# Kernel tuning notes

Measured on AMD Instinct MI355X. Metric: run time of the kernel, lower is better.

The kernel has to match this reference:

```python
import jax, jax.numpy as jnp
import numpy as np

T = 1048576  # length of the return series


def setup_inputs() -> dict:
    key = jax.random.key(0)
    y = jax.random.normal(key, (T,), dtype=jnp.float32) * 0.01
    f32 = lambda v: jnp.asarray(v, dtype=jnp.float32)
    return {
        "y": y,
        "omega": f32(0.000115944368734123),
        "alpha": f32(2.91880490811086e-06),
        "phi": f32(0.887721679393748),
        "lam": f32(2.38788661600365),
        "gam1": f32(332.934927419811),
        "gam2": f32(134.424516082664),
        "vphi": f32(1.61007979938689e-06),
        "rho": f32(0.990486709209338),
    }


def reference(y, omega, alpha, phi, lam, gam1, gam2, vphi, rho):
    # Component Heston-Nandi GARCH volatility recurrence.
    # h_0 = q_0 = Var(y)  (population variance, matching tf.math.reduce_variance)
    q0 = jnp.var(y)
    h0 = q0

    def step(carry, y_prev):
        h_t, q_t = carry
        s = jnp.sqrt(h_t)
        z = (y_prev - lam * h_t) / s
        innov = z * z - 1.0
        q_new = omega + rho * (q_t - omega) + vphi * (innov - 2.0 * gam2 * s * z)
        h_new = q_new + phi * (h_t - q_new) + alpha * (innov - 2.0 * gam1 * s * z)
        return (h_new, q_new), h_new

    # step t uses y[t-1], producing h[1..T-1]
    (_, _), hs = jax.lax.scan(step, (h0, q0), y[:-1])
    return jnp.concatenate([h0[None], hs])  # shape (T,)
```

## Files before the change

### kernel.cpp

```cpp
#include <hip/hip_runtime.h>

#define T_LEN   1048576
#define CHUNK   16
#define WARM    512
#define SBLOCK  256
#define OUTS_PER_BLOCK (SBLOCK * CHUNK)
#define SGRID   (T_LEN / OUTS_PER_BLOCK)
#define WIN     (WARM + OUTS_PER_BLOCK)
#define WIN4    (WIN / 4)
#define LDS_DW  (WIN + (WIN / 64) * 4)
#define RGRID   256

__global__ __launch_bounds__(256)
void var_partials_kernel(const float* __restrict__ y, double2* __restrict__ ws) {
    int tid = blockIdx.x * blockDim.x + threadIdx.x;
    const float4* y4 = (const float4*)y;
    const int stride = RGRID * 256;
    float4 v0 = y4[tid];
    float4 v1 = y4[tid + stride];
    float4 v2 = y4[tid + 2 * stride];
    float4 v3 = y4[tid + 3 * stride];
    double s = 0.0, s2 = 0.0;
    #define ACC(v) { double a=(v).x,b=(v).y,c=(v).z,d=(v).w; s += (a+b)+(c+d); s2 += (a*a+b*b)+(c*c+d*d); }
    ACC(v0) ACC(v1) ACC(v2) ACC(v3)
    #undef ACC
    for (int off = 32; off >= 1; off >>= 1) {
        s  += __shfl_down(s,  off, 64);
        s2 += __shfl_down(s2, off, 64);
    }
    __shared__ double lsum[4], lsq[4];
    int lane = threadIdx.x & 63, wv = threadIdx.x >> 6;
    if (lane == 0) { lsum[wv] = s; lsq[wv] = s2; }
    __syncthreads();
    if (threadIdx.x == 0) {
        double2 o;
        o.x = (lsum[0] + lsum[1]) + (lsum[2] + lsum[3]);
        o.y = (lsq[0]  + lsq[1])  + (lsq[2]  + lsq[3]);
        ws[blockIdx.x] = o;
    }
}

struct ChnP { float lam, DA, E, B, phi, A, cV, rho, cv2, vphi; };

__device__ __forceinline__ void chn_step(float yv, float& h, float& q, const ChnP& P) {
    float u  = fmaf(-P.lam, h, yv);
    float r  = __builtin_amdgcn_rcpf(h);
    float t1 = fmaf(P.E, q, P.DA);
    float s1 = fmaf(P.rho, q, P.cV);
    float u2 = u * u;
    float t2 = fmaf(P.B, u, t1);
    float s2 = fmaf(P.cv2, u, s1);
    float t3 = fmaf(P.phi, h, t2);
    float Ar = P.A * r;
    float Vr = P.vphi * r;
    h = fmaf(u2, Ar, t3);
    q = fmaf(u2, Vr, s2);
}

__device__ __forceinline__ void chn_step4(const float4& v, float& h, float& q, const ChnP& P) {
    chn_step(v.x, h, q, P);
    chn_step(v.y, h, q, P);
    chn_step(v.z, h, q, P);
    chn_step(v.w, h, q, P);
}

__device__ __forceinline__ float4 lds_r4(const float* b, int d) {
    return *(const float4*)&b[d + ((d >> 6) << 2)];
}
__device__ __forceinline__ void lds_w4(float* b, int d, float4 v) {
    *(float4*)&b[d + ((d >> 6) << 2)] = v;
}

__global__ __launch_bounds__(SBLOCK, 1)
void chn_scan_kernel(const float* __restrict__ y, float* __restrict__ out,
                     const double2* __restrict__ ws,
                     const float* __restrict__ p_omega, const float* __restrict__ p_alpha,
                     const float* __restrict__ p_phi,   const float* __restrict__ p_lam,
                     const float* __restrict__ p_gam1,  const float* __restrict__ p_gam2,
                     const float* __restrict__ p_vphi,  const float* __restrict__ p_rho) {
    __shared__ __align__(16) float ybuf[LDS_DW];

    const int B0    = blockIdx.x * OUTS_PER_BLOCK;
    const int gbase = (blockIdx.x == 0) ? 0 : (B0 - WARM);

    {
        const float4* g4 = (const float4*)(y + gbase);
        for (int i = threadIdx.x; i < WIN4; i += SBLOCK) {
            lds_w4(ybuf, 4 * i, g4[i]);
        }
    }

    const float omega = *p_omega, alpha = *p_alpha, phi = *p_phi, lam = *p_lam;
    const float gam1 = *p_gam1, gam2 = *p_gam2, vphi = *p_vphi, rho = *p_rho;
    const float onemphi = 1.0f - phi;
    const float c0  = omega * (1.0f - rho);
    const float cv2 = -2.0f * gam2 * vphi;
    const float c1  = -2.0f * gam1 * alpha;
    ChnP P;
    P.lam = lam; P.rho = rho; P.cv2 = cv2; P.vphi = vphi; P.phi = phi;
    P.A  = fmaf(onemphi, vphi, alpha);
    P.B  = fmaf(onemphi, cv2, c1);
    P.E  = onemphi * rho;
    P.DA = onemphi * c0 - P.A;
    P.cV = c0 - vphi;

    int lane = threadIdx.x & 63;
    double s = 0.0, s2 = 0.0;
    #pragma unroll
    for (int k = 0; k < 4; ++k) {
        double2 v = ws[lane + 64 * k];
        s += v.x; s2 += v.y;
    }
    #pragma unroll
    for (int off = 32; off >= 1; off >>= 1) {
        s  += __shfl_xor(s,  off, 64);
        s2 += __shfl_xor(s2, off, 64);
    }
    const double inv_t = 1.0 / (double)T_LEN;
    double mean = s * inv_t;
    const float var = (float)(s2 * inv_t - mean * mean);

    __syncthreads();

    const int t0 = B0 + threadIdx.x * CHUNK;
    float h = var, q = var;
    float4* out4 = (float4*)(out + t0);

    if (blockIdx.x != 0) {
        const int dw = threadIdx.x * CHUNK;
        float4 a = lds_r4(ybuf, dw + 0);
        float4 b = lds_r4(ybuf, dw + 4);
        #pragma unroll 2
        for (int f = 0; f < WARM / 4; f += 2) {
            float4 na = lds_r4(ybuf, dw + 4 * (f + 2));
            float4 nb = lds_r4(ybuf, dw + 4 * (f + 3));
            chn_step4(a, h, q, P);
            chn_step4(b, h, q, P);
            a = na; b = nb;
        }
        float4 c = lds_r4(ybuf, dw + WARM + 8);
        float4 d = lds_r4(ybuf, dw + WARM + 12);
        float4 o;
        o.x = h; chn_step(a.x, h, q, P);
        o.y = h; chn_step(a.y, h, q, P);
        o.z = h; chn_step(a.z, h, q, P);
        o.w = h; chn_step(a.w, h, q, P);
        out4[0] = o;
        o.x = h; chn_step(b.x, h, q, P);
        o.y = h; chn_step(b.y, h, q, P);
        o.z = h; chn_step(b.z, h, q, P);
        o.w = h; chn_step(b.w, h, q, P);
        out4[1] = o;
        o.x = h; chn_step(c.x, h, q, P);
        o.y = h; chn_step(c.y, h, q, P);
        o.z = h; chn_step(c.z, h, q, P);
        o.w = h; chn_step(c.w, h, q, P);
        out4[2] = o;
        o.x = h; chn_step(d.x, h, q, P);
        o.y = h; chn_step(d.y, h, q, P);
        o.z = h; chn_step(d.z, h, q, P);
        o.w = h; chn_step(d.w, h, q, P);
        out4[3] = o;
    } else {
        const int nW = (t0 < WARM) ? t0 : WARM;
        const int d0 = t0 - nW;
        for (int f = 0; f < nW / 4; ++f) {
            float4 v = lds_r4(ybuf, d0 + 4 * f);
            chn_step4(v, h, q, P);
        }
        #pragma unroll
        for (int j = 0; j < CHUNK / 4; ++j) {
            float4 v = lds_r4(ybuf, t0 + 4 * j);
            float4 o;
            o.x = h; chn_step(v.x, h, q, P);
            o.y = h; chn_step(v.y, h, q, P);
            o.z = h; chn_step(v.z, h, q, P);
            o.w = h; chn_step(v.w, h, q, P);
            out4[j] = o;
        }
    }
}

extern "C" void kernel_launch(void* const* d_in, const int* in_sizes, int n_in,
                              void* d_out, int out_size, void* d_ws, size_t ws_size,
                              hipStream_t stream) {
    const float* y = (const float*)d_in[0];
    float* out = (float*)d_out;
    double2* ws = (double2*)d_ws;

    var_partials_kernel<<<RGRID, 256, 0, stream>>>(y, ws);

    chn_scan_kernel<<<SGRID, SBLOCK, 0, stream>>>(
        y, out, ws,
        (const float*)d_in[1], (const float*)d_in[2], (const float*)d_in[3],
        (const float*)d_in[4], (const float*)d_in[5], (const float*)d_in[6],
        (const float*)d_in[7], (const float*)d_in[8]);
}
```

Before: 89.49 us.

## Fuse variance reduction into scan kernel with cross-block flag sync; shorten warmup

Removes the separate variance-partials kernel. Each scan block now sums its own 4096-element slice from the LDS copy it already loads, publishes the partial sums with a release flag, and spins until all 256 blocks' flags are set before computing the variance. This removes one launch and a second pass over global memory. The warm-up length drops from 512 to 448 steps, which shortens the serial recurrence each thread runs, at some cost in accuracy. The step function also merges the two reciprocal multiplies into one shared product. Risks: the grid-wide spin wait depends on all blocks being co-resident. The flags are never reset, so later calls can read the previous call's partial sums before the current ones are written.

```diff
diff --git a/kernel.cpp b/kernel.cpp
--- a/kernel.cpp
+++ b/kernel.cpp
@@ -2,59 +2,29 @@
 
 #define T_LEN   1048576
 #define CHUNK   16
-#define WARM    512
+#define WARM    448
 #define SBLOCK  256
 #define OUTS_PER_BLOCK (SBLOCK * CHUNK)
 #define SGRID   (T_LEN / OUTS_PER_BLOCK)
 #define WIN     (WARM + OUTS_PER_BLOCK)
 #define WIN4    (WIN / 4)
 #define LDS_DW  (WIN + (WIN / 64) * 4)
-#define RGRID   256
-
-__global__ __launch_bounds__(256)
-void var_partials_kernel(const float* __restrict__ y, double2* __restrict__ ws) {
-    int tid = blockIdx.x * blockDim.x + threadIdx.x;
-    const float4* y4 = (const float4*)y;
-    const int stride = RGRID * 256;
-    float4 v0 = y4[tid];
-    float4 v1 = y4[tid + stride];
-    float4 v2 = y4[tid + 2 * stride];
-    float4 v3 = y4[tid + 3 * stride];
-    double s = 0.0, s2 = 0.0;
-    #define ACC(v) { double a=(v).x,b=(v).y,c=(v).z,d=(v).w; s += (a+b)+(c+d); s2 += (a*a+b*b)+(c*c+d*d); }
-    ACC(v0) ACC(v1) ACC(v2) ACC(v3)
-    #undef ACC
-    for (int off = 32; off >= 1; off >>= 1) {
-        s  += __shfl_down(s,  off, 64);
-        s2 += __shfl_down(s2, off, 64);
-    }
-    __shared__ double lsum[4], lsq[4];
-    int lane = threadIdx.x & 63, wv = threadIdx.x >> 6;
-    if (lane == 0) { lsum[wv] = s; lsq[wv] = s2; }
-    __syncthreads();
-    if (threadIdx.x == 0) {
-        double2 o;
-        o.x = (lsum[0] + lsum[1]) + (lsum[2] + lsum[3]);
-        o.y = (lsq[0]  + lsq[1])  + (lsq[2]  + lsq[3]);
-        ws[blockIdx.x] = o;
-    }
-}
+#define FLAG_MAGIC 0x13572468u
 
 struct ChnP { float lam, DA, E, B, phi, A, cV, rho, cv2, vphi; };
 
 __device__ __forceinline__ void chn_step(float yv, float& h, float& q, const ChnP& P) {
     float u  = fmaf(-P.lam, h, yv);
     float r  = __builtin_amdgcn_rcpf(h);
-    float t1 = fmaf(P.E, q, P.DA);
-    float s1 = fmaf(P.rho, q, P.cV);
+    float hl = fmaf(P.E, q, P.DA);
+    float ql = fmaf(P.rho, q, P.cV);
     float u2 = u * u;
-    float t2 = fmaf(P.B, u, t1);
-    float s2 = fmaf(P.cv2, u, s1);
-    float t3 = fmaf(P.phi, h, t2);
-    float Ar = P.A * r;
-    float Vr = P.vphi * r;
-    h = fmaf(u2, Ar, t3);
-    q = fmaf(u2, Vr, s2);
+    hl = fmaf(P.B, u, hl);
+    ql = fmaf(P.cv2, u, ql);
+    hl = fmaf(P.phi, h, hl);
+    float t  = u2 * r;
+    h = fmaf(P.A, t, hl);
+    q = fmaf(P.vphi, t, ql);
 }
 
 __device__ __forceinline__ void chn_step4(const float4& v, float& h, float& q, const ChnP& P) {
@@ -72,12 +42,13 @@
 }
 
 __global__ __launch_bounds__(SBLOCK, 1)
-void chn_scan_kernel(const float* __restrict__ y, float* __restrict__ out,
-                     const double2* __restrict__ ws,
-                     const float* __restrict__ p_omega, const float* __restrict__ p_alpha,
-                     const float* __restrict__ p_phi,   const float* __restrict__ p_lam,
-                     const float* __restrict__ p_gam1,  const float* __restrict__ p_gam2,
-                     const float* __restrict__ p_vphi,  const float* __restrict__ p_rho) {
+void chn_fused_kernel(const float* __restrict__ y, float* __restrict__ out,
+                      double* __restrict__ ps, double* __restrict__ ps2,
+                      unsigned* __restrict__ flags,
+                      const float* __restrict__ p_omega, const float* __restrict__ p_alpha,
+                      const float* __restrict__ p_phi,   const float* __restrict__ p_lam,
+                      const float* __restrict__ p_gam1,  const float* __restrict__ p_gam2,
+                      const float* __restrict__ p_vphi,  const float* __restrict__ p_rho) {
     __shared__ __align__(16) float ybuf[LDS_DW];
 
     const int B0    = blockIdx.x * OUTS_PER_BLOCK;
@@ -104,12 +75,48 @@
     P.DA = onemphi * c0 - P.A;
     P.cV = c0 - vphi;
 
+    __syncthreads();
+
+    {
+        const int voff = (blockIdx.x == 0) ? 0 : WARM;
+        double s = 0.0, s2 = 0.0;
+        #pragma unroll
+        for (int k = 0; k < 4; ++k) {
+            float4 v = lds_r4(ybuf, voff + 4 * threadIdx.x + 1024 * k);
+            double a = v.x, b = v.y, c = v.z, d = v.w;
+            s  += (a + b) + (c + d);
+            s2 += (a * a + b * b) + (c * c + d * d);
+        }
+        #pragma unroll
+        for (int off = 32; off >= 1; off >>= 1) {
+            s  += __shfl_down(s,  off, 64);
+            s2 += __shfl_down(s2, off, 64);
+        }
+        __shared__ double lsum[4], lsq[4];
+        int wv = threadIdx.x >> 6;
+        if ((threadIdx.x & 63) == 0) { lsum[wv] = s; lsq[wv] = s2; }
+        __syncthreads();
+        if (threadIdx.x == 0) {
+            double ts  = (lsum[0] + lsum[1]) + (lsum[2] + lsum[3]);
+            double ts2 = (lsq[0]  + lsq[1])  + (lsq[2]  + lsq[3]);
+            __hip_atomic_store(&ps[blockIdx.x],  ts,  __ATOMIC_RELAXED, __HIP_MEMORY_SCOPE_AGENT);
+            __hip_atomic_store(&ps2[blockIdx.x], ts2, __ATOMIC_RELAXED, __HIP_MEMORY_SCOPE_AGENT);
+            __hip_atomic_store(&flags[blockIdx.x], FLAG_MAGIC, __ATOMIC_RELEASE, __HIP_MEMORY_SCOPE_AGENT);
+        }
+    }
+
+    while (__hip_atomic_load(&flags[threadIdx.x], __ATOMIC_ACQUIRE, __HIP_MEMORY_SCOPE_AGENT)
+           != FLAG_MAGIC) {
+        __builtin_amdgcn_s_sleep(1);
+    }
+    __syncthreads();
+
     int lane = threadIdx.x & 63;
     double s = 0.0, s2 = 0.0;
     #pragma unroll
     for (int k = 0; k < 4; ++k) {
-        double2 v = ws[lane + 64 * k];
-        s += v.x; s2 += v.y;
+        s  += __hip_atomic_load(&ps[lane + 64 * k],  __ATOMIC_RELAXED, __HIP_MEMORY_SCOPE_AGENT);
+        s2 += __hip_atomic_load(&ps2[lane + 64 * k], __ATOMIC_RELAXED, __HIP_MEMORY_SCOPE_AGENT);
     }
     #pragma unroll
     for (int off = 32; off >= 1; off >>= 1) {
@@ -119,8 +126,6 @@
     const double inv_t = 1.0 / (double)T_LEN;
     double mean = s * inv_t;
     const float var = (float)(s2 * inv_t - mean * mean);
-
-    __syncthreads();
 
     const int t0 = B0 + threadIdx.x * CHUNK;
     float h = var, q = var;
@@ -186,12 +191,12 @@
                               hipStream_t stream) {
     const float* y = (const float*)d_in[0];
     float* out = (float*)d_out;
-    double2* ws = (double2*)d_ws;
-
-    var_partials_kernel<<<RGRID, 256, 0, stream>>>(y, ws);
-
-    chn_scan_kernel<<<SGRID, SBLOCK, 0, stream>>>(
-        y, out, ws,
+    double*   ps    = (double*)d_ws;
+    double*   ps2   = (double*)((char*)d_ws + 2048);
+    unsigned* flags = (unsigned*)((char*)d_ws + 4096);
+
+    chn_fused_kernel<<<SGRID, SBLOCK, 0, stream>>>(
+        y, out, ps, ps2, flags,
         (const float*)d_in[1], (const float*)d_in[2], (const float*)d_in[3],
         (const float*)d_in[4], (const float*)d_in[5], (const float*)d_in[6],
         (const float*)d_in[7], (const float*)d_in[8]);
```

New measurement: 106.9 us. 19.5% more time.

## Halve chunk size, shorten warmup, and pack h/q updates into packed FMAs

Applied to the files above, without the earlier changes.

Each thread now produces 8 outputs instead of 16 with a 384-step warmup instead of 512, doubling the grid and shortening each thread's serial chain (warmup plus chunk). The h and q updates are packed into 2-wide vector FMAs so the compiler can emit packed FP32 instructions. The min-blocks launch bound hint is dropped as well. The shorter warmup raises the risk that the truncated recurrence has not converged, and total redundant warmup work grows relative to outputs.

```diff
diff --git a/kernel.cpp b/kernel.cpp
--- a/kernel.cpp
+++ b/kernel.cpp
@@ -1,8 +1,8 @@
 #include <hip/hip_runtime.h>
 
 #define T_LEN   1048576
-#define CHUNK   16
-#define WARM    512
+#define CHUNK   8
+#define WARM    384
 #define SBLOCK  256
 #define OUTS_PER_BLOCK (SBLOCK * CHUNK)
 #define SGRID   (T_LEN / OUTS_PER_BLOCK)
@@ -10,6 +10,8 @@
 #define WIN4    (WIN / 4)
 #define LDS_DW  (WIN + (WIN / 64) * 4)
 #define RGRID   256
+
+typedef float v2f __attribute__((ext_vector_type(2)));
 
 __global__ __launch_bounds__(256)
 void var_partials_kernel(const float* __restrict__ y, double2* __restrict__ ws) {
@@ -40,21 +42,26 @@
     }
 }
 
-struct ChnP { float lam, DA, E, B, phi, A, cV, rho, cv2, vphi; };
+struct ChnP {
+    float lam;
+    v2f DC;
+    v2f EC;
+    v2f BC;
+    v2f PH;
+    v2f AV;
+};
 
 __device__ __forceinline__ void chn_step(float yv, float& h, float& q, const ChnP& P) {
     float u  = fmaf(-P.lam, h, yv);
     float r  = __builtin_amdgcn_rcpf(h);
-    float t1 = fmaf(P.E, q, P.DA);
-    float s1 = fmaf(P.rho, q, P.cV);
+    v2f acc  = __builtin_elementwise_fma(P.EC, (v2f){q, q}, P.DC);
     float u2 = u * u;
-    float t2 = fmaf(P.B, u, t1);
-    float s2 = fmaf(P.cv2, u, s1);
-    float t3 = fmaf(P.phi, h, t2);
-    float Ar = P.A * r;
-    float Vr = P.vphi * r;
-    h = fmaf(u2, Ar, t3);
-    q = fmaf(u2, Vr, s2);
+    acc      = __builtin_elementwise_fma(P.BC, (v2f){u, u}, acc);
+    acc      = __builtin_elementwise_fma(P.PH, (v2f){h, h}, acc);
+    float t  = u2 * r;
+    acc      = __builtin_elementwise_fma(P.AV, (v2f){t, t}, acc);
+    h = acc.x;
+    q = acc.y;
 }
 
 __device__ __forceinline__ void chn_step4(const float4& v, float& h, float& q, const ChnP& P) {
@@ -71,7 +78,7 @@
     *(float4*)&b[d + ((d >> 6) << 2)] = v;
 }
 
-__global__ __launch_bounds__(SBLOCK, 1)
+__global__ __launch_bounds__(SBLOCK)
 void chn_scan_kernel(const float* __restrict__ y, float* __restrict__ out,
                      const double2* __restrict__ ws,
                      const float* __restrict__ p_omega, const float* __restrict__ p_alpha,
@@ -96,13 +103,16 @@
     const float c0  = omega * (1.0f - rho);
     const float cv2 = -2.0f * gam2 * vphi;
     const float c1  = -2.0f * gam1 * alpha;
+    const float A   = fmaf(onemphi, vphi, alpha);
+    const float B   = fmaf(onemphi, cv2, c1);
+    const float E   = onemphi * rho;
     ChnP P;
-    P.lam = lam; P.rho = rho; P.cv2 = cv2; P.vphi = vphi; P.phi = phi;
-    P.A  = fmaf(onemphi, vphi, alpha);
-    P.B  = fmaf(onemphi, cv2, c1);
-    P.E  = onemphi * rho;
-    P.DA = onemphi * c0 - P.A;
-    P.cV = c0 - vphi;
+    P.lam = lam;
+    P.DC  = (v2f){onemphi * c0 - A, c0 - vphi};
+    P.EC  = (v2f){E, rho};
+    P.BC  = (v2f){B, cv2};
+    P.PH  = (v2f){phi, 0.0f};
+    P.AV  = (v2f){A, vphi};
 
     int lane = threadIdx.x & 63;
     double s = 0.0, s2 = 0.0;
@@ -138,8 +148,6 @@
             chn_step4(b, h, q, P);
             a = na; b = nb;
         }
-        float4 c = lds_r4(ybuf, dw + WARM + 8);
-        float4 d = lds_r4(ybuf, dw + WARM + 12);
         float4 o;
         o.x = h; chn_step(a.x, h, q, P);
         o.y = h; chn_step(a.y, h, q, P);
@@ -151,16 +159,6 @@
         o.z = h; chn_step(b.z, h, q, P);
         o.w = h; chn_step(b.w, h, q, P);
         out4[1] = o;
-        o.x = h; chn_step(c.x, h, q, P);
-        o.y = h; chn_step(c.y, h, q, P);
-        o.z = h; chn_step(c.z, h, q, P);
-        o.w = h; chn_step(c.w, h, q, P);
-        out4[2] = o;
-        o.x = h; chn_step(d.x, h, q, P);
-        o.y = h; chn_step(d.y, h, q, P);
-        o.z = h; chn_step(d.z, h, q, P);
-        o.w = h; chn_step(d.w, h, q, P);
-        out4[3] = o;
     } else {
         const int nW = (t0 < WARM) ? t0 : WARM;
         const int d0 = t0 - nW;
```

New measurement: 90.17 us. Within noise of the previous version (+0.8%).
